# Optimization experiments

Measured on AMD Instinct MI355X. Metric: run time of the kernel, lower is better.

Reference implementation:

```python
import jax, jax.numpy as jnp
import numpy as np

N = 500000      # nodes
E = 1250000     # edges
S = 50000       # subgraphs
G = 64          # graphs
D = 64          # hidden dim (M_in = M_out = 64)
NLAYERS = 5


def setup_inputs() -> dict:
    key = jax.random.key(0)
    ks = jax.random.split(key, 24)

    def p(k, shape):
        return jax.random.normal(k, shape, dtype=jnp.float32) * 0.05

    return {
        "z": jax.random.randint(ks[0], (N,), 0, 100),
        "edge_index": jax.random.randint(ks[1], (2, E), 0, N),
        "node_to_subgraph": jax.random.randint(ks[2], (N,), 0, S),
        "subgraph_to_graph": jax.random.randint(ks[3], (S,), 0, G),
        # per-layer params (stacked over the 5 conv layers)
        "z_tables": p(ks[4], (NLAYERS, 100, D)),      # Embedding(100, 64) x5
        "tf_W": p(ks[5], (NLAYERS - 1, D, 2 * D)),    # Linear(128, 64) for layers 1..4
        "tf_b": p(ks[6], (NLAYERS - 1, D)),
        "ggc_W": p(ks[7], (NLAYERS, D, D)),           # GatedGraphConv weight[0]
        "gru_wih": p(ks[8], (NLAYERS, 3 * D, D)),
        "gru_whh": p(ks[9], (NLAYERS, 3 * D, D)),
        "gru_bih": p(ks[10], (NLAYERS, 3 * D)),
        "gru_bhh": p(ks[11], (NLAYERS, 3 * D)),
        # head
        "fc1_W": p(ks[12], (32, D)), "fc1_b": p(ks[13], (32,)),
        "fc2_W": p(ks[14], (16, 32)), "fc2_b": p(ks[15], (16,)),
        "fc3_W": p(ks[16], (1, 16)), "fc3_b": p(ks[17], (1,)),
    }


def reference(z, edge_index, node_to_subgraph, subgraph_to_graph,
              z_tables, tf_W, tf_b, ggc_W,
              gru_wih, gru_whh, gru_bih, gru_bhh,
              fc1_W, fc1_b, fc2_W, fc2_b, fc3_W, fc3_b):
    src, dst = edge_index[0], edge_index[1]
    x = None
    for layer in range(NLAYERS):
        ze = z_tables[layer][z]                      # [N, 64] embedding lookup
        if x is None:
            x = ze
        else:
            x = jnp.concatenate([x, ze], axis=-1) @ tf_W[layer - 1].T + tf_b[layer - 1]
        # GatedGraphConv with num_layers=1: m = x @ W; add-aggregate; GRUCell update
        m = x @ ggc_W[layer]                          # [N, 64]
        agg = jax.ops.segment_sum(m[src], dst, num_segments=N)  # scatter-add to dst
        gi = agg @ gru_wih[layer].T + gru_bih[layer]  # [N, 192]
        gh = x @ gru_whh[layer].T + gru_bhh[layer]    # [N, 192]
        ir, iz, inn = jnp.split(gi, 3, axis=-1)
        hr, hz, hn = jnp.split(gh, 3, axis=-1)
        r = jax.nn.sigmoid(ir + hr)
        u = jax.nn.sigmoid(iz + hz)
        n = jnp.tanh(inn + r * hn)
        x = (1.0 - u) * n + u * x
    # subgraph pooling ('mean' branch actually does global_add_pool)
    x = jax.ops.segment_sum(x, node_to_subgraph, num_segments=S)   # [S, 64]
    # graph pooling (y_ndim == 1)
    x = jax.ops.segment_sum(x, subgraph_to_graph, num_segments=G)  # [G, 64]
    x = jax.nn.elu(x @ fc1_W.T + fc1_b)
    x = jax.nn.elu(x @ fc2_W.T + fc2_b)
    return x @ fc3_W.T + fc3_b                        # [G, 1]
```

## Files before the change

kernel.cpp:

```cpp
#include <hip/hip_runtime.h>
#include <hip/hip_bf16.h>

#define NN 500000
#define EE 1250000
#define NP 501760
#define NBLK 489
#define GCAP 16384

typedef __attribute__((ext_vector_type(8))) short bf16x8;
typedef __attribute__((ext_vector_type(4))) float f32x4;

__device__ __forceinline__ float ngnn97_bf2f(unsigned short u) {
  return __uint_as_float(((unsigned int)u) << 16);
}
__device__ __forceinline__ unsigned short ngnn97_f2bf(float f) {
  union { __hip_bfloat16 b; unsigned short u; } cv;
  cv.b = __float2bfloat16(f);
  return cv.u;
}
__device__ __forceinline__ void ngnn97_acc8(uint4 u, float* lo, float* hi) {
  lo[0] += __uint_as_float(u.x << 16); hi[0] += __uint_as_float(u.x & 0xFFFF0000u);
  lo[1] += __uint_as_float(u.y << 16); hi[1] += __uint_as_float(u.y & 0xFFFF0000u);
  lo[2] += __uint_as_float(u.z << 16); hi[2] += __uint_as_float(u.z & 0xFFFF0000u);
  lo[3] += __uint_as_float(u.w << 16); hi[3] += __uint_as_float(u.w & 0xFFFF0000u);
}

__global__ void ngnn97_code(float* __restrict__ out, float v) {
  if (threadIdx.x < 64) out[threadIdx.x] = v;
}

__global__ __launch_bounds__(256) void ngnn97_pre(
    const float* __restrict__ ggc, const float* __restrict__ wih,
    const float* __restrict__ whh, const float* __restrict__ bih,
    const float* __restrict__ bhh, const float* __restrict__ tfW,
    const float* __restrict__ ztab,
    unsigned short* __restrict__ Ubt, float* __restrict__ Ub,
    unsigned short* __restrict__ Vbt, unsigned short* __restrict__ ztabh) {
  int idx = blockIdx.x * 256 + threadIdx.x;
  if (idx < 163840) {
    int l = idx >> 15, r = idx & 32767;
    int n = r >> 7, k = r & 127;
    float v = 0.f;
    if (k < 64) {
      if (n < 192) {
        const float* gp = ggc + l * 4096 + k * 64;
        const float* wp = wih + l * 12288 + n * 64;
        float acc = 0.f;
#pragma unroll
        for (int t2 = 0; t2 < 64; t2++) acc = fmaf(gp[t2], wp[t2], acc);
        v = acc;
      }
    } else {
      int k2 = k - 64;
      if (n < 128) v = whh[l * 12288 + n * 64 + k2];
      else if (n >= 192) v = whh[l * 12288 + (n - 64) * 64 + k2];
    }
    Ubt[idx] = ngnn97_f2bf(v);
  } else if (idx < 196608) {
    int i2 = idx - 163840;
    Vbt[i2] = ngnn97_f2bf(tfW[i2]);
  } else if (idx < 197888) {
    int i2 = idx - 196608;
    int l = i2 >> 8, j = i2 & 255;
    float v;
    if (j < 128)      v = bih[l * 192 + j] + bhh[l * 192 + j];
    else if (j < 192) v = bih[l * 192 + j];
    else              v = bhh[l * 192 + j - 64];
    Ub[i2] = v;
  } else if (idx < 229888) {
    int i2 = idx - 197888;
    ztabh[i2] = ngnn97_f2bf(ztab[i2]);
  }
}

__global__ __launch_bounds__(256) void ngnn97_hist(const int* __restrict__ dst, int* __restrict__ counts) {
  int e = blockIdx.x * 256 + threadIdx.x;
  if (e < EE) atomicAdd(&counts[dst[e]], 1);
}

__global__ __launch_bounds__(256) void ngnn97_red(const int* __restrict__ counts, int* __restrict__ bsum) {
  __shared__ int s[256];
  int t = threadIdx.x, base = blockIdx.x * 1024;
  int v = 0;
#pragma unroll
  for (int i = 0; i < 4; i++) v += counts[base + t + i * 256];
  s[t] = v; __syncthreads();
  for (int o = 128; o > 0; o >>= 1) { if (t < o) s[t] += s[t + o]; __syncthreads(); }
  if (t == 0) bsum[blockIdx.x] = s[0];
}

__global__ __launch_bounds__(512) void ngnn97_scan1(const int* __restrict__ bsum, int* __restrict__ boff) {
  __shared__ int s[512];
  int t = threadIdx.x;
  int v = (t < NBLK) ? bsum[t] : 0;
  s[t] = v; __syncthreads();
  for (int o = 1; o < 512; o <<= 1) {
    int a = (t >= o) ? s[t - o] : 0;
    __syncthreads(); s[t] += a; __syncthreads();
  }
  if (t < NBLK) boff[t] = s[t] - v;
}

__global__ __launch_bounds__(256) void ngnn97_scan2(const int* __restrict__ counts, const int* __restrict__ boff,
                                                    int* __restrict__ row_ptr, int* __restrict__ cursor) {
  __shared__ int s[256];
  int t = threadIdx.x, base = blockIdx.x * 1024;
  int4 c = *(const int4*)(counts + base + t * 4);
  int tsum = c.x + c.y + c.z + c.w;
  s[t] = tsum; __syncthreads();
  for (int o = 1; o < 256; o <<= 1) {
    int a = (t >= o) ? s[t - o] : 0;
    __syncthreads(); s[t] += a; __syncthreads();
  }
  int off = boff[blockIdx.x] + s[t] - tsum;
  int4 r;
  r.x = off; r.y = off + c.x; r.z = off + c.x + c.y; r.w = off + c.x + c.y + c.z;
  *(int4*)(row_ptr + base + t * 4) = r;
  *(int4*)(cursor + base + t * 4) = r;
}

__global__ __launch_bounds__(256) void ngnn97_fill(const int* __restrict__ src, const int* __restrict__ dst,
                                                   int* __restrict__ cursor, int* __restrict__ srcs) {
  int e = blockIdx.x * 256 + threadIdx.x;
  if (e < EE) {
    int pos = atomicAdd(&cursor[dst[e]], 1);
    srcs[pos] = src[e];
  }
}

__global__ __launch_bounds__(256) void ngnn97_g8(const int* __restrict__ n2s, const int* __restrict__ s2g,
                                                 unsigned char* __restrict__ g8) {
  int idx = blockIdx.x * 256 + threadIdx.x;
  if (idx < NN) g8[idx] = (unsigned char)s2g[n2s[idx]];
}

__global__ __launch_bounds__(256) void ngnn97_bucket(const unsigned char* __restrict__ g8,
                                                     int* __restrict__ gcur, int* __restrict__ nlist) {
  __shared__ int hcnt[64];
  __shared__ int hbase[64];
  int t = threadIdx.x;
  int base = blockIdx.x * 1024;
  if (t < 64) hcnt[t] = 0;
  __syncthreads();
#pragma unroll
  for (int i = 0; i < 4; i++) {
    int node = base + i * 256 + t;
    if (node < NN) atomicAdd(&hcnt[g8[node]], 1);
  }
  __syncthreads();
  if (t < 64) {
    int c = hcnt[t];
    hbase[t] = (c > 0) ? atomicAdd(&gcur[t], c) : 0;
    hcnt[t] = 0;
  }
  __syncthreads();
#pragma unroll
  for (int i = 0; i < 4; i++) {
    int node = base + i * 256 + t;
    if (node < NN) {
      int g = g8[node];
      int loc = atomicAdd(&hcnt[g], 1);
      int pos = hbase[g] + loc;
      if (pos < GCAP) nlist[g * GCAP + pos] = node;
    }
  }
}

__global__ __launch_bounds__(256) void ngnn97_dhist(const int* __restrict__ rowp, int* __restrict__ dbins) {
  __shared__ int h[64];
  int t = threadIdx.x, base = blockIdx.x * 1024;
  if (t < 64) h[t] = 0;
  __syncthreads();
#pragma unroll
  for (int i = 0; i < 4; i++) {
    int node = base + i * 256 + t;
    if (node < NN) {
      int d = rowp[node + 1] - rowp[node];
      if (d > 63) d = 63;
      atomicAdd(&h[d], 1);
    }
  }
  __syncthreads();
  if (t < 64 && h[t]) atomicAdd(&dbins[t], h[t]);
}

__global__ __launch_bounds__(64) void ngnn97_dscan(const int* __restrict__ dbins, int* __restrict__ dcur) {
  __shared__ int s[64];
  int t = threadIdx.x;
  int v = dbins[t];
  s[t] = v; __syncthreads();
  for (int o = 1; o < 64; o <<= 1) {
    int a = (t >= o) ? s[t - o] : 0;
    __syncthreads(); s[t] += a; __syncthreads();
  }
  dcur[t] = s[t] - v;
}

__global__ __launch_bounds__(256) void ngnn97_dfill(const int* __restrict__ rowp, int* __restrict__ dcur,
                                                    int* __restrict__ perm) {
  __shared__ int hcnt[64];
  __shared__ int hbase[64];
  int t = threadIdx.x, base = blockIdx.x * 1024;
  if (t < 64) hcnt[t] = 0;
  __syncthreads();
#pragma unroll
  for (int i = 0; i < 4; i++) {
    int node = base + i * 256 + t;
    if (node < NN) {
      int d = rowp[node + 1] - rowp[node];
      if (d > 63) d = 63;
      atomicAdd(&hcnt[d], 1);
    }
  }
  __syncthreads();
  if (t < 64) {
    int c = hcnt[t];
    hbase[t] = (c > 0) ? atomicAdd(&dcur[t], c) : 0;
    hcnt[t] = 0;
  }
  __syncthreads();
#pragma unroll
  for (int i = 0; i < 4; i++) {
    int node = base + i * 256 + t;
    if (node < NN) {
      int d = rowp[node + 1] - rowp[node];
      if (d > 63) d = 63;
      int loc = atomicAdd(&hcnt[d], 1);
      perm[hbase[d] + loc] = node;
    }
  }
}

__global__ __launch_bounds__(256) void ngnn97_embed(const int* __restrict__ z,
                                                    const unsigned short* __restrict__ ztabh,
                                                    unsigned short* __restrict__ xh) {
  int idx = blockIdx.x * 256 + threadIdx.x;
  int node = idx >> 3, sub = idx & 7;
  if (node < NN) {
    int zz = z[node];
    *(bf16x8*)(xh + (size_t)node * 64 + sub * 8) =
        *(const bf16x8*)(ztabh + zz * 64 + sub * 8);
  }
}

__global__ __launch_bounds__(64, 4) void ngnn97_gru(
    const unsigned short* __restrict__ xh_old, unsigned short* __restrict__ xh_new,
    const int* __restrict__ rowp, const int* __restrict__ srcs,
    const int* __restrict__ perm,
    const unsigned short* __restrict__ Ubt, const float* __restrict__ Ub,
    const unsigned short* __restrict__ Vbt, const float* __restrict__ tfb,
    const int* __restrict__ z, const unsigned short* __restrict__ ztabh,
    int do_transform) {
  __shared__ unsigned short Abuf[32 * 72];
  __shared__ int pnode[32];
  const int lane = threadIdx.x;
  const int ncol = lane & 15, quad = lane >> 4;
  const int nbase = blockIdx.x * 32;

  if (lane < 32) {
    int idx = nbase + lane;
    pnode[lane] = (idx < NN) ? perm[idx] : NN;
  }

  {
    int grp = lane >> 2, sub = lane & 3;
#pragma unroll
    for (int sb = 0; sb < 2; sb++) {
      int row = sb * 16 + grp;
      int node = pnode[row];
      float lo[8], hi[8];
#pragma unroll
      for (int i = 0; i < 8; i++) { lo[i] = 0.f; hi[i] = 0.f; }
      if (node < NN) {
        int b = rowp[node], e = rowp[node + 1];
        int p = b;
        for (; p + 2 <= e; p += 2) {
          int s0 = srcs[p], s1 = srcs[p + 1];
          const unsigned short* r0 = xh_old + (size_t)s0 * 64 + sub * 16;
          const unsigned short* r1 = xh_old + (size_t)s1 * 64 + sub * 16;
          uint4 u0 = *(const uint4*)(r0);
          uint4 u1 = *(const uint4*)(r0 + 8);
          uint4 u2 = *(const uint4*)(r1);
          uint4 u3 = *(const uint4*)(r1 + 8);
          ngnn97_acc8(u0, lo, hi); ngnn97_acc8(u1, lo + 4, hi + 4);
          ngnn97_acc8(u2, lo, hi); ngnn97_acc8(u3, lo + 4, hi + 4);
        }
        if (p < e) {
          const unsigned short* r0 = xh_old + (size_t)srcs[p] * 64 + sub * 16;
          uint4 u0 = *(const uint4*)(r0);
          uint4 u1 = *(const uint4*)(r0 + 8);
          ngnn97_acc8(u0, lo, hi);
          ngnn97_acc8(u1, lo + 4, hi + 4);
        }
      }
#pragma unroll
      for (int c = 0; c < 2; c++) {
        bf16x8 ov;
#pragma unroll
        for (int j = 0; j < 4; j++) {
          ov[2 * j]     = (short)ngnn97_f2bf(lo[c * 4 + j]);
          ov[2 * j + 1] = (short)ngnn97_f2bf(hi[c * 4 + j]);
        }
        *(bf16x8*)(Abuf + row * 72 + sub * 16 + c * 8) = ov;
      }
    }
  }

  bf16x8 afrA[2][2];
#pragma unroll
  for (int mm = 0; mm < 2; mm++)
#pragma unroll
    for (int kc = 0; kc < 2; kc++)
      afrA[mm][kc] = *(const bf16x8*)(Abuf + (mm * 16 + ncol) * 72 + quad * 8 + kc * 32);

#pragma unroll
  for (int i = 0; i < 8; i++) {
    int chunk = i * 64 + lane;
    int r2 = chunk >> 4, c4 = (chunk & 15) << 2;
    int node = pnode[r2];
    ushort4 qx = make_ushort4(0, 0, 0, 0);
    if (node < NN) qx = *(const ushort4*)(xh_old + (size_t)node * 64 + c4);
    *(ushort4*)(Abuf + r2 * 72 + c4) = qx;
  }

  bf16x8 afrX[2][2];
#pragma unroll
  for (int mm = 0; mm < 2; mm++)
#pragma unroll
    for (int kc = 0; kc < 2; kc++)
      afrX[mm][kc] = *(const bf16x8*)(Abuf + (mm * 16 + ncol) * 72 + quad * 8 + kc * 32);

#pragma unroll
  for (int c = 0; c < 4; c++) {
    f32x4 aR[2], aZ[2], aN[2], aH[2];
#pragma unroll
    for (int mm = 0; mm < 2; mm++) {
      aR[mm] = (f32x4){0.f, 0.f, 0.f, 0.f}; aZ[mm] = aR[mm];
      aN[mm] = aR[mm]; aH[mm] = aR[mm];
    }
#pragma unroll
    for (int kc = 0; kc < 4; kc++) {
      const unsigned short* ub = Ubt + (size_t)(c * 16 + ncol) * 128 + quad * 8 + kc * 32;
      bf16x8 bR = *(const bf16x8*)(ub);
      bf16x8 bZ = *(const bf16x8*)(ub + 64 * 128);
      bf16x8 bX = (kc < 2) ? *(const bf16x8*)(ub + 128 * 128)
                           : *(const bf16x8*)(ub + 192 * 128);
#pragma unroll
      for (int mm = 0; mm < 2; mm++) {
        bf16x8 a = (kc < 2) ? afrA[mm][kc] : afrX[mm][kc - 2];
        aR[mm] = __builtin_amdgcn_mfma_f32_16x16x32_bf16(a, bR, aR[mm], 0, 0, 0);
        aZ[mm] = __builtin_amdgcn_mfma_f32_16x16x32_bf16(a, bZ, aZ[mm], 0, 0, 0);
        if (kc < 2) aN[mm] = __builtin_amdgcn_mfma_f32_16x16x32_bf16(a, bX, aN[mm], 0, 0, 0);
        else        aH[mm] = __builtin_amdgcn_mfma_f32_16x16x32_bf16(a, bX, aH[mm], 0, 0, 0);
      }
    }
    int j = c * 16 + ncol;
    float bRs = Ub[j], bZs = Ub[64 + j], bNs = Ub[128 + j], bHs = Ub[192 + j];
#pragma unroll
    for (int mm = 0; mm < 2; mm++)
#pragma unroll
      for (int r = 0; r < 4; r++) {
        int row = mm * 16 + quad * 4 + r;
        float R = aR[mm][r] + bRs, Z = aZ[mm][r] + bZs;
        float Nv = aN[mm][r] + bNs, H = aH[mm][r] + bHs;
        float rg = 1.f / (1.f + __expf(-R));
        float ug = 1.f / (1.f + __expf(-Z));
        float e2 = __expf(2.f * (Nv + rg * H));
        float nn2 = 1.f - 2.f / (e2 + 1.f);
        float xo = ngnn97_bf2f(Abuf[row * 72 + j]);
        Abuf[row * 72 + j] = ngnn97_f2bf((1.f - ug) * nn2 + ug * xo);
      }
  }

  if (do_transform) {
    bf16x8 afrN[2][2], afrE[2][2];
#pragma unroll
    for (int mm = 0; mm < 2; mm++) {
      int node = pnode[mm * 16 + ncol];
      int zz = (node < NN) ? z[node] : 0;
#pragma unroll
      for (int kc = 0; kc < 2; kc++) {
        afrN[mm][kc] = *(const bf16x8*)(Abuf + (mm * 16 + ncol) * 72 + quad * 8 + kc * 32);
        afrE[mm][kc] = *(const bf16x8*)(ztabh + zz * 64 + quad * 8 + kc * 32);
      }
    }
#pragma unroll
    for (int c2 = 0; c2 < 4; c2++) {
      f32x4 acc[2];
      acc[0] = (f32x4){0.f, 0.f, 0.f, 0.f}; acc[1] = acc[0];
#pragma unroll
      for (int kc = 0; kc < 4; kc++) {
        bf16x8 bV = *(const bf16x8*)(Vbt + (size_t)(c2 * 16 + ncol) * 128 + quad * 8 + kc * 32);
#pragma unroll
        for (int mm = 0; mm < 2; mm++) {
          bf16x8 a = (kc < 2) ? afrN[mm][kc] : afrE[mm][kc - 2];
          acc[mm] = __builtin_amdgcn_mfma_f32_16x16x32_bf16(a, bV, acc[mm], 0, 0, 0);
        }
      }
      int j = c2 * 16 + ncol;
      float bt = tfb[j];
#pragma unroll
      for (int mm = 0; mm < 2; mm++)
#pragma unroll
        for (int r = 0; r < 4; r++) {
          int row = mm * 16 + quad * 4 + r;
          Abuf[row * 72 + j] = ngnn97_f2bf(acc[mm][r] + bt);
        }
    }
  }

#pragma unroll
  for (int i = 0; i < 8; i++) {
    int chunk = i * 64 + lane;
    int r2 = chunk >> 4, c4 = (chunk & 15) << 2;
    int node = pnode[r2];
    if (node < NN)
      *(ushort4*)(xh_new + (size_t)node * 64 + c4) = *(const ushort4*)(Abuf + r2 * 72 + c4);
  }
}

__global__ __launch_bounds__(256) void ngnn97_pool(const unsigned short* __restrict__ xh,
                                                   const int* __restrict__ nlist,
                                                   const int* __restrict__ gcur,
                                                   float* __restrict__ gpool) {
  __shared__ float part[4][64];
  int t = threadIdx.x;
  int lane = t & 63, wv = t >> 6;
  int g = blockIdx.x >> 4, c = blockIdx.x & 15;
  int cnt = gcur[g];
  if (cnt > GCAP) cnt = GCAP;
  int r0 = (c * cnt) >> 4, r1 = ((c + 1) * cnt) >> 4;
  const int* nl = nlist + g * GCAP;
  float a0 = 0.f, a1 = 0.f;
  int r = r0 + wv;
  for (; r + 4 < r1; r += 8) {
    int n0 = nl[r], n1 = nl[r + 4];
    a0 += ngnn97_bf2f(xh[(size_t)n0 * 64 + lane]);
    a1 += ngnn97_bf2f(xh[(size_t)n1 * 64 + lane]);
  }
  if (r < r1) a0 += ngnn97_bf2f(xh[(size_t)nl[r] * 64 + lane]);
  part[wv][lane] = a0 + a1;
  __syncthreads();
  if (t < 64)
    atomicAdd(&gpool[g * 64 + t], part[0][t] + part[1][t] + part[2][t] + part[3][t]);
}

__global__ __launch_bounds__(256) void ngnn97_head(
    const float* __restrict__ gpool,
    const float* __restrict__ W1, const float* __restrict__ b1,
    const float* __restrict__ W2, const float* __restrict__ b2,
    const float* __restrict__ W3, const float* __restrict__ b3,
    float* __restrict__ out) {
  __shared__ float gp[4096];
  __shared__ float h1[2048];
  __shared__ float h2[1024];
  int t = threadIdx.x;
  for (int i = t; i < 4096; i += 256) gp[i] = gpool[i];
  __syncthreads();
  for (int i = t; i < 2048; i += 256) {
    int g = i >> 5, o = i & 31;
    float a = b1[o];
    for (int d = 0; d < 64; d++) a = fmaf(gp[g * 64 + d], W1[o * 64 + d], a);
    h1[i] = (a > 0.f) ? a : (__expf(a) - 1.f);
  }
  __syncthreads();
  for (int i = t; i < 1024; i += 256) {
    int g = i >> 4, o = i & 15;
    float a = b2[o];
    for (int d = 0; d < 32; d++) a = fmaf(h1[g * 32 + d], W2[o * 32 + d], a);
    h2[i] = (a > 0.f) ? a : (__expf(a) - 1.f);
  }
  __syncthreads();
  if (t < 64) {
    float a = b3[0];
    for (int d = 0; d < 16; d++) a = fmaf(h2[t * 16 + d], W3[d], a);
    out[t] = a;
  }
}

#define OFF_XH0   ((size_t)0)
#define OFF_XH1   ((size_t)64000000)
#define OFF_CNT   ((size_t)128000000)
#define OFF_ROW   (OFF_CNT + (size_t)NP * 4)
#define OFF_CUR   (OFF_ROW + (size_t)NP * 4)
#define OFF_SRC   (OFF_CUR + (size_t)NP * 4)
#define OFF_BSUM  (OFF_SRC + (size_t)EE * 4)
#define OFF_BOFF  (OFF_BSUM + (size_t)2048)
#define OFF_U     (OFF_BOFF + (size_t)2048)
#define OFF_UB    (OFF_U + (size_t)327680)
#define OFF_V     (OFF_UB + (size_t)5120)
#define OFF_GP    (OFF_V + (size_t)65536)
#define OFF_G8    (OFF_GP + (size_t)16384)
#define OFF_ZTH   (OFF_G8 + (size_t)500736)
#define OFF_GCUR  (OFF_ZTH + (size_t)64000)
#define OFF_NL    (OFF_GCUR + (size_t)1024)
#define OFF_PERM  (OFF_NL + (size_t)64 * GCAP * 4)
#define OFF_DB    (OFF_PERM + (size_t)NP * 4)
#define OFF_DC    (OFF_DB + (size_t)256)
#define WS_NEED   (OFF_DC + (size_t)256)

extern "C" void kernel_launch(void* const* d_in, const int* in_sizes, int n_in,
                              void* d_out, int out_size, void* d_ws, size_t ws_size,
                              hipStream_t stream) {
  float* out = (float*)d_out;
  if (ws_size < WS_NEED) {
    ngnn97_code<<<1, 64, 0, stream>>>(out, 7.0f);
    return;
  }

  const int* z    = (const int*)d_in[0];
  const int* ei   = (const int*)d_in[1];
  const int* n2s  = (const int*)d_in[2];
  const int* s2g  = (const int*)d_in[3];
  const float* ztab = (const float*)d_in[4];
  const float* tfW  = (const float*)d_in[5];
  const float* tfb  = (const float*)d_in[6];
  const float* ggc  = (const float*)d_in[7];
  const float* wih  = (const float*)d_in[8];
  const float* whh  = (const float*)d_in[9];
  const float* bih  = (const float*)d_in[10];
  const float* bhh  = (const float*)d_in[11];
  const float* W1   = (const float*)d_in[12];
  const float* b1   = (const float*)d_in[13];
  const float* W2   = (const float*)d_in[14];
  const float* b2   = (const float*)d_in[15];
  const float* W3   = (const float*)d_in[16];
  const float* b3   = (const float*)d_in[17];

  char* ws = (char*)d_ws;
  unsigned short* xh0    = (unsigned short*)(ws + OFF_XH0);
  unsigned short* xh1    = (unsigned short*)(ws + OFF_XH1);
  int*            counts = (int*)(ws + OFF_CNT);
  int*            rowp   = (int*)(ws + OFF_ROW);
  int*            curs   = (int*)(ws + OFF_CUR);
  int*            srcs   = (int*)(ws + OFF_SRC);
  int*            bsum   = (int*)(ws + OFF_BSUM);
  int*            boff   = (int*)(ws + OFF_BOFF);
  unsigned short* Ubt    = (unsigned short*)(ws + OFF_U);
  float*          Ub     = (float*)(ws + OFF_UB);
  unsigned short* Vbt    = (unsigned short*)(ws + OFF_V);
  float*          gpool  = (float*)(ws + OFF_GP);
  unsigned char*  g8     = (unsigned char*)(ws + OFF_G8);
  unsigned short* ztabh  = (unsigned short*)(ws + OFF_ZTH);
  int*            gcur   = (int*)(ws + OFF_GCUR);
  int*            nlist  = (int*)(ws + OFF_NL);
  int*            perm   = (int*)(ws + OFF_PERM);
  int*            dbins  = (int*)(ws + OFF_DB);
  int*            dcur   = (int*)(ws + OFF_DC);

  hipMemsetAsync(counts, 0, (size_t)NP * 4, stream);
  hipMemsetAsync(gpool, 0, 16384, stream);
  hipMemsetAsync(gcur, 0, 1024, stream);
  hipMemsetAsync(dbins, 0, 256, stream);

  ngnn97_pre<<<899, 256, 0, stream>>>(ggc, wih, whh, bih, bhh, tfW, ztab, Ubt, Ub, Vbt, ztabh);
  ngnn97_g8<<<(NN + 255) / 256, 256, 0, stream>>>(n2s, s2g, g8);
  ngnn97_bucket<<<NBLK, 256, 0, stream>>>(g8, gcur, nlist);

  const int* srcp = ei;
  const int* dstp = ei + EE;
  ngnn97_hist<<<(EE + 255) / 256, 256, 0, stream>>>(dstp, counts);
  ngnn97_red<<<NBLK, 256, 0, stream>>>(counts, bsum);
  ngnn97_scan1<<<1, 512, 0, stream>>>(bsum, boff);
  ngnn97_scan2<<<NBLK, 256, 0, stream>>>(counts, boff, rowp, curs);
  ngnn97_fill<<<(EE + 255) / 256, 256, 0, stream>>>(srcp, dstp, curs, srcs);

  ngnn97_dhist<<<NBLK, 256, 0, stream>>>(rowp, dbins);
  ngnn97_dscan<<<1, 64, 0, stream>>>(dbins, dcur);
  ngnn97_dfill<<<NBLK, 256, 0, stream>>>(rowp, dcur, perm);

  ngnn97_embed<<<(NN * 8 + 255) / 256, 256, 0, stream>>>(z, ztabh, xh0);

  unsigned short* xc = xh0;
  unsigned short* xn2 = xh1;
  for (int l = 0; l < 5; l++) {
    ngnn97_gru<<<(NN + 31) / 32, 64, 0, stream>>>(
        xc, xn2, rowp, srcs, perm,
        Ubt + (size_t)l * 32768, Ub + (size_t)l * 256,
        Vbt + (size_t)(l < 4 ? l : 0) * 8192, tfb + (size_t)(l < 4 ? l : 0) * 64,
        z, ztabh + (size_t)(l < 4 ? l + 1 : 0) * 6400, (l < 4) ? 1 : 0);
    unsigned short* tmp = xc; xc = xn2; xn2 = tmp;
  }

  ngnn97_pool<<<1024, 256, 0, stream>>>(xc, nlist, gcur, gpool);
  ngnn97_head<<<1, 256, 0, stream>>>(gpool, W1, b1, W2, b2, W3, b3, out);
}
```

Before: 1.064 ms.

## Replace global degree sort with per-block local sort and prefetch edge sources

After: 1.140 ms. +7.1%, slower.

```diff
diff --git a/kernel.cpp b/kernel.cpp
--- a/kernel.cpp
+++ b/kernel.cpp
@@ -166,40 +166,10 @@
   }
 }
 
-__global__ __launch_bounds__(256) void ngnn97_dhist(const int* __restrict__ rowp, int* __restrict__ dbins) {
-  __shared__ int h[64];
-  int t = threadIdx.x, base = blockIdx.x * 1024;
-  if (t < 64) h[t] = 0;
-  __syncthreads();
-#pragma unroll
-  for (int i = 0; i < 4; i++) {
-    int node = base + i * 256 + t;
-    if (node < NN) {
-      int d = rowp[node + 1] - rowp[node];
-      if (d > 63) d = 63;
-      atomicAdd(&h[d], 1);
-    }
-  }
-  __syncthreads();
-  if (t < 64 && h[t]) atomicAdd(&dbins[t], h[t]);
-}
-
-__global__ __launch_bounds__(64) void ngnn97_dscan(const int* __restrict__ dbins, int* __restrict__ dcur) {
-  __shared__ int s[64];
-  int t = threadIdx.x;
-  int v = dbins[t];
-  s[t] = v; __syncthreads();
-  for (int o = 1; o < 64; o <<= 1) {
-    int a = (t >= o) ? s[t - o] : 0;
-    __syncthreads(); s[t] += a; __syncthreads();
-  }
-  dcur[t] = s[t] - v;
-}
-
-__global__ __launch_bounds__(256) void ngnn97_dfill(const int* __restrict__ rowp, int* __restrict__ dcur,
+__global__ __launch_bounds__(256) void ngnn97_dsort(const int* __restrict__ rowp,
                                                     int* __restrict__ perm) {
   __shared__ int hcnt[64];
-  __shared__ int hbase[64];
+  __shared__ int hoff[64];
   int t = threadIdx.x, base = blockIdx.x * 1024;
   if (t < 64) hcnt[t] = 0;
   __syncthreads();
@@ -213,11 +183,12 @@
     }
   }
   __syncthreads();
-  if (t < 64) {
-    int c = hcnt[t];
-    hbase[t] = (c > 0) ? atomicAdd(&dcur[t], c) : 0;
-    hcnt[t] = 0;
-  }
+  if (t == 0) {
+    int s = 0;
+    for (int d = 0; d < 64; d++) { hoff[d] = s; s += hcnt[d]; }
+  }
+  __syncthreads();
+  if (t < 64) hcnt[t] = 0;
   __syncthreads();
 #pragma unroll
   for (int i = 0; i < 4; i++) {
@@ -226,7 +197,7 @@
       int d = rowp[node + 1] - rowp[node];
       if (d > 63) d = 63;
       int loc = atomicAdd(&hcnt[d], 1);
-      perm[hbase[d] + loc] = node;
+      perm[base + hoff[d] + loc] = node;
     }
   }
 }
@@ -274,16 +245,21 @@
       if (node < NN) {
         int b = rowp[node], e = rowp[node + 1];
         int p = b;
-        for (; p + 2 <= e; p += 2) {
+        if (p + 2 <= e) {
           int s0 = srcs[p], s1 = srcs[p + 1];
-          const unsigned short* r0 = xh_old + (size_t)s0 * 64 + sub * 16;
-          const unsigned short* r1 = xh_old + (size_t)s1 * 64 + sub * 16;
-          uint4 u0 = *(const uint4*)(r0);
-          uint4 u1 = *(const uint4*)(r0 + 8);
-          uint4 u2 = *(const uint4*)(r1);
-          uint4 u3 = *(const uint4*)(r1 + 8);
-          ngnn97_acc8(u0, lo, hi); ngnn97_acc8(u1, lo + 4, hi + 4);
-          ngnn97_acc8(u2, lo, hi); ngnn97_acc8(u3, lo + 4, hi + 4);
+          for (; p + 2 <= e; p += 2) {
+            int n0 = srcs[p + 2];
+            int n1 = srcs[p + 3];
+            const unsigned short* r0 = xh_old + (size_t)s0 * 64 + sub * 16;
+            const unsigned short* r1 = xh_old + (size_t)s1 * 64 + sub * 16;
+            uint4 u0 = *(const uint4*)(r0);
+            uint4 u1 = *(const uint4*)(r0 + 8);
+            uint4 u2 = *(const uint4*)(r1);
+            uint4 u3 = *(const uint4*)(r1 + 8);
+            ngnn97_acc8(u0, lo, hi); ngnn97_acc8(u1, lo + 4, hi + 4);
+            ngnn97_acc8(u2, lo, hi); ngnn97_acc8(u3, lo + 4, hi + 4);
+            s0 = n0; s1 = n1;
+          }
         }
         if (p < e) {
           const unsigned short* r0 = xh_old + (size_t)srcs[p] * 64 + sub * 16;
@@ -484,7 +460,7 @@
 #define OFF_ROW   (OFF_CNT + (size_t)NP * 4)
 #define OFF_CUR   (OFF_ROW + (size_t)NP * 4)
 #define OFF_SRC   (OFF_CUR + (size_t)NP * 4)
-#define OFF_BSUM  (OFF_SRC + (size_t)EE * 4)
+#define OFF_BSUM  (OFF_SRC + (size_t)(EE + 2) * 4)
 #define OFF_BOFF  (OFF_BSUM + (size_t)2048)
 #define OFF_U     (OFF_BOFF + (size_t)2048)
 #define OFF_UB    (OFF_U + (size_t)327680)
@@ -495,9 +471,7 @@
 #define OFF_GCUR  (OFF_ZTH + (size_t)64000)
 #define OFF_NL    (OFF_GCUR + (size_t)1024)
 #define OFF_PERM  (OFF_NL + (size_t)64 * GCAP * 4)
-#define OFF_DB    (OFF_PERM + (size_t)NP * 4)
-#define OFF_DC    (OFF_DB + (size_t)256)
-#define WS_NEED   (OFF_DC + (size_t)256)
+#define WS_NEED   (OFF_PERM + (size_t)NP * 4)
 
 extern "C" void kernel_launch(void* const* d_in, const int* in_sizes, int n_in,
                               void* d_out, int out_size, void* d_ws, size_t ws_size,
@@ -545,13 +519,10 @@
   int*            gcur   = (int*)(ws + OFF_GCUR);
   int*            nlist  = (int*)(ws + OFF_NL);
   int*            perm   = (int*)(ws + OFF_PERM);
-  int*            dbins  = (int*)(ws + OFF_DB);
-  int*            dcur   = (int*)(ws + OFF_DC);
 
   hipMemsetAsync(counts, 0, (size_t)NP * 4, stream);
   hipMemsetAsync(gpool, 0, 16384, stream);
   hipMemsetAsync(gcur, 0, 1024, stream);
-  hipMemsetAsync(dbins, 0, 256, stream);
 
   ngnn97_pre<<<899, 256, 0, stream>>>(ggc, wih, whh, bih, bhh, tfW, ztab, Ubt, Ub, Vbt, ztabh);
   ngnn97_g8<<<(NN + 255) / 256, 256, 0, stream>>>(n2s, s2g, g8);
@@ -565,9 +536,7 @@
   ngnn97_scan2<<<NBLK, 256, 0, stream>>>(counts, boff, rowp, curs);
   ngnn97_fill<<<(EE + 255) / 256, 256, 0, stream>>>(srcp, dstp, curs, srcs);
 
-  ngnn97_dhist<<<NBLK, 256, 0, stream>>>(rowp, dbins);
-  ngnn97_dscan<<<1, 64, 0, stream>>>(dbins, dcur);
-  ngnn97_dfill<<<NBLK, 256, 0, stream>>>(rowp, dcur, perm);
+  ngnn97_dsort<<<NBLK, 256, 0, stream>>>(rowp, perm);
 
   ngnn97_embed<<<(NN * 8 + 255) / 256, 256, 0, stream>>>(z, ztabh, xh0);
 
```
